# Kernel optimization log

Measured on AMD Instinct MI355X. Metric: run time of the kernel, lower is better.

Reference implementation:

```python
import jax, jax.numpy as jnp
import numpy as np

JACCARD_THRESH = 0.5
NEG_POS = 3
VAR0, VAR1 = 0.1, 0.2
MAX_POS = 256  # static cap on gathered positives for the metric-learning terms


def point_form(boxes):
    # (cx,cy,w,h) -> (xmin,ymin,xmax,ymax)
    return jnp.concatenate([boxes[:, :2] - boxes[:, 2:] / 2,
                            boxes[:, :2] + boxes[:, 2:] / 2], axis=1)


def jaccard(a, b):
    # a: [O,4], b: [D,4] point form
    lt = jnp.maximum(a[:, None, :2], b[None, :, :2])
    rb = jnp.minimum(a[:, None, 2:], b[None, :, 2:])
    wh = jnp.clip(rb - lt, 0.0)
    inter = wh[..., 0] * wh[..., 1]
    area_a = (a[:, 2] - a[:, 0]) * (a[:, 3] - a[:, 1])
    area_b = (b[:, 2] - b[:, 0]) * (b[:, 3] - b[:, 1])
    return inter / (area_a[:, None] + area_b[None, :] - inter)


def encode(matched, priors):
    g_cxcy = ((matched[:, :2] + matched[:, 2:]) / 2 - priors[:, :2]) / (VAR0 * priors[:, 2:])
    g_wh = jnp.log((matched[:, 2:] - matched[:, :2]) / priors[:, 2:]) / VAR1
    return jnp.concatenate([g_cxcy, g_wh], axis=1)


def match_one(truths, labels, poses, priors):
    # standard SSD match (per image)
    ov = jaccard(truths, point_form(priors))          # [O, D]
    best_prior_idx = jnp.argmax(ov, axis=1)           # [O]
    best_truth_ov = jnp.max(ov, axis=0)               # [D]
    best_truth_idx = jnp.argmax(ov, axis=0)           # [D]
    best_truth_ov = best_truth_ov.at[best_prior_idx].set(2.0)
    best_truth_idx = best_truth_idx.at[best_prior_idx].set(jnp.arange(truths.shape[0]))
    matches = truths[best_truth_idx]                  # [D,4]
    conf = labels[best_truth_idx] + 1                 # background=0
    conf = jnp.where(best_truth_ov < JACCARD_THRESH, 0, conf)
    return encode(matches, priors), conf.astype(jnp.int32), poses[best_truth_idx]


def multibox_loss(loc_data, conf_data, line_data, pose_data, dbox_list, targets):
    B, D, C = conf_data.shape
    truths = targets[:, :, 0:4]
    labels = targets[:, :, 4].astype(jnp.int32)
    poses = targets[:, :, 5:8]
    loc_t, conf_t, pose_t = jax.vmap(match_one, in_axes=(0, 0, 0, None))(
        truths, labels, poses, dbox_list)

    pos = conf_t > 0                                  # [B,D]
    posf = pos.astype(loc_data.dtype)

    # smooth-L1 loc loss over positives (sum reduction)
    d = loc_data - loc_t
    sl1 = jnp.where(jnp.abs(d) < 1.0, 0.5 * d * d, jnp.abs(d) - 0.5)
    loss_l = jnp.sum(sl1 * posf[..., None])

    # pose squared-error over positives
    loss_p = jnp.sum((pose_data - pose_t) ** 2 * posf[..., None])

    # per-anchor cross entropy + hard-negative mining (double-argsort rank trick)
    logp = jax.nn.log_softmax(conf_data, axis=-1)
    ce = -jnp.take_along_axis(logp, conf_t[..., None], axis=-1)[..., 0]  # [B,D]
    ce_mined = jnp.where(pos, 0.0, ce)
    loss_idx = jnp.argsort(-ce_mined, axis=1)
    idx_rank = jnp.argsort(loss_idx, axis=1)
    num_pos = jnp.sum(pos.astype(jnp.int32), axis=1, keepdims=True)
    num_neg = jnp.minimum(num_pos * NEG_POS, D)
    neg = idx_rank < num_neg
    loss_c = jnp.sum(ce * (pos | neg).astype(ce.dtype))

    N = jnp.maximum(jnp.sum(posf), 1.0)
    loss_l = loss_l / N
    loss_c = loss_c / N
    loss_p = loss_p / N

    # ---- metric-learning block on gathered positives (static cap) ----
    pos_flat = pos.reshape(-1)
    order = jnp.argsort(jnp.where(pos_flat, 0, 1))[:MAX_POS]  # stable: row-major positives first
    valid = pos_flat[order]                                   # [K]
    emb = line_data.reshape(-1, line_data.shape[-1])[order]   # [K,32] raw embeddings
    lab = conf_t.reshape(-1)[order]                           # [K]
    qp = pose_t.reshape(-1, 3)[order]                         # [K,3]

    # PairMarginMiner / TripletMarginLoss use L2-normalized LpDistance by default
    nemb = emb / jnp.maximum(jnp.linalg.norm(emb, axis=1, keepdims=True), 1e-12)
    sq = jnp.sum((nemb[:, None, :] - nemb[None, :, :]) ** 2, axis=-1)
    dist = jnp.sqrt(jnp.maximum(sq, 1e-12))                   # [K,K]

    K = emb.shape[0]
    eye = jnp.eye(K, dtype=bool)
    vpair = valid[:, None] & valid[None, :] & ~eye
    same = lab[:, None] == lab[None, :]
    pos_pair = vpair & same & (dist > 0.2)   # mined hard positive pairs
    neg_pair = vpair & ~same & (dist < 0.8)  # mined hard negative pairs
    n_pp = jnp.sum(pos_pair)
    n_np = jnp.sum(neg_pair)

    # pairs -> triplets sharing the anchor; TripletMarginLoss(margin=0.2), AvgNonZero reducer
    trip_mask = pos_pair[:, :, None] & neg_pair[:, None, :]           # [K,K,K]
    trip_loss = jax.nn.relu(dist[:, :, None] - dist[:, None, :] + 0.2)
    nz = trip_mask & (trip_loss > 0)
    loss_t = jnp.sum(jnp.where(nz, trip_loss, 0.0)) / jnp.maximum(jnp.sum(nz), 1)

    # Ldesk over mined positive pairs: raw-embedding sq-dist vs pose sq-dist consistency
    e_sq = jnp.sum((emb[:, None, :] - emb[None, :, :]) ** 2, axis=-1)
    q_sq = jnp.sum((qp[:, None, :] - qp[None, :, :]) ** 2, axis=-1)
    desk_sum = jnp.sum(jnp.where(pos_pair, (e_sq - q_sq) ** 2, 0.0))
    npp = jnp.maximum(n_pp, 1).astype(loc_data.dtype)
    Ldesk = desk_sum / npp + loss_t / jnp.maximum(n_pp + n_np, 1)
    Ldesk = Ldesk / npp / 32.0

    return loss_l, loss_c, loss_p, Ldesk, loss_t


def setup_inputs():
    key = jax.random.key(0)
    ks = jax.random.split(key, 10)
    B, D, C, L, O = 32, 8732, 21, 32, 8
    loc_data = jax.random.normal(ks[0], (B, D, 4)) * 0.1
    conf_data = jax.random.normal(ks[1], (B, D, C))
    line_data = jax.random.normal(ks[2], (B, D, L))
    pose_data = jax.random.normal(ks[3], (B, D, 3))
    # default boxes (cx,cy,w,h) in (0,1)
    cxcy = jax.random.uniform(ks[4], (D, 2), minval=0.05, maxval=0.95)
    wh = jax.random.uniform(ks[5], (D, 2), minval=0.05, maxval=0.4)
    dbox_list = jnp.concatenate([cxcy, wh], axis=1)
    # targets: [xmin,ymin,xmax,ymax,label,pose(3),unused]
    mins = jax.random.uniform(ks[6], (B, O, 2), minval=0.0, maxval=0.6)
    sizes = jax.random.uniform(ks[7], (B, O, 2), minval=0.1, maxval=0.4)
    boxes = jnp.concatenate([mins, mins + sizes], axis=-1)
    labs = jax.random.randint(ks[8], (B, O, 1), 0, C - 1).astype(jnp.float32)
    pz = jax.random.normal(ks[9], (B, O, 3))
    targets = jnp.concatenate([boxes, labs, pz, jnp.zeros((B, O, 1))], axis=-1)
    return dict(loc_data=loc_data, conf_data=conf_data, line_data=line_data,
                pose_data=pose_data, dbox_list=dbox_list, targets=targets)


def reference(loc_data, conf_data, line_data, pose_data, dbox_list, targets):
    return multibox_loss(loc_data, conf_data, line_data, pose_data, dbox_list, targets)
```

## Files before the change

### kernel.cpp

```cpp
#include <hip/hip_runtime.h>
#include <cstdint>

#define B 32
#define D 8732
#define C 21
#define L 32
#define O 8
#define NS 8
#define SLICE 1092
#define NT 1024

struct Ws {
  const float *loc, *conf, *line, *pose, *dbox, *targets;
  float* out;
  int* cnt;
  int* posSlice;
  float* sce;
  double *gLossL, *gLossP, *gCeP;
  double *gCeNeg;
  double *gDesk, *gNpp, *gNnp, *gTripS, *gTripC;
};

__device__ inline double waveSumD(double v) {
  #pragma unroll
  for (int s = 32; s > 0; s >>= 1) v += __shfl_down(v, s, 64);
  return v;
}

__device__ inline float iou_one(float tx1, float ty1, float tx2, float ty2, float ta,
                                float px1, float py1, float px2, float py2, float areaB) {
  float lx = fmaxf(tx1, px1), ly = fmaxf(ty1, py1);
  float rx = fminf(tx2, px2), ry = fminf(ty2, py2);
  float iw = fmaxf(rx - lx, 0.f), ih = fmaxf(ry - ly, 0.f);
  float inter = iw * ih;
  return inter / (ta + areaB - inter);
}

struct Sh1 {
  float tb[O][4], ta[O], tl[O], tp_[O][3];
  unsigned long long wm[16][O];
  int bpd[O];
  int plist[256];
  int wcnt[16], wbase[16];
  double wred[16][3];
  int run;
};

__global__ __launch_bounds__(NT) void k_match(Ws p) {
  __shared__ Sh1 sh;
  int g = blockIdx.x, tid = threadIdx.x;
  int lane = tid & 63, wav = tid >> 6;
  int b = g >> 3, s = g & 7;
  int dBeg = s * SLICE;
  int dEnd = dBeg + SLICE; if (dEnd > D) dEnd = D;

  if (tid < O) {
    const float* tr = p.targets + ((size_t)b * O + tid) * 9;
    sh.tb[tid][0] = tr[0]; sh.tb[tid][1] = tr[1];
    sh.tb[tid][2] = tr[2]; sh.tb[tid][3] = tr[3];
    sh.ta[tid] = (tr[2] - tr[0]) * (tr[3] - tr[1]);
    sh.tl[tid] = tr[4];
    sh.tp_[tid][0] = tr[5]; sh.tp_[tid][1] = tr[6]; sh.tp_[tid][2] = tr[7];
  }
  if (tid == 0) sh.run = 0;
  __syncthreads();

  {
    unsigned long long key[O];
    #pragma unroll
    for (int t = 0; t < O; t++) key[t] = 0ull;
    for (int d = tid; d < D; d += NT) {
      float4 db = *(const float4*)(p.dbox + (size_t)d * 4);
      float px1 = db.x - 0.5f*db.z, py1 = db.y - 0.5f*db.w;
      float px2 = db.x + 0.5f*db.z, py2 = db.y + 0.5f*db.w;
      float areaB = db.z * db.w;
      #pragma unroll
      for (int t = 0; t < O; t++) {
        float iou = iou_one(sh.tb[t][0], sh.tb[t][1], sh.tb[t][2], sh.tb[t][3],
                            sh.ta[t], px1, py1, px2, py2, areaB);
        unsigned long long kk = ((unsigned long long)__float_as_uint(iou) << 32)
                              | (unsigned long long)(0xFFFFFFFFu - (unsigned)d);
        if (kk > key[t]) key[t] = kk;
      }
    }
    #pragma unroll
    for (int t = 0; t < O; t++) {
      unsigned long long k = key[t];
      #pragma unroll
      for (int sft = 32; sft > 0; sft >>= 1) {
        unsigned long long o = __shfl_down(k, sft, 64);
        if (o > k) k = o;
      }
      if (lane == 0) sh.wm[wav][t] = k;
    }
    __syncthreads();
    if (tid < O) {
      unsigned long long k = sh.wm[0][tid];
      #pragma unroll
      for (int w = 1; w < 16; w++) if (sh.wm[w][tid] > k) k = sh.wm[w][tid];
      sh.bpd[tid] = (int)(0xFFFFFFFFu - (unsigned)(k & 0xFFFFFFFFull));
    }
    __syncthreads();
  }

  const unsigned long long lt = (lane == 0) ? 0ull : (~0ull >> (64 - lane));
  double ll = 0, lp = 0, cp = 0;
  for (int d0 = dBeg; d0 < dEnd; d0 += NT) {
    int d = d0 + tid;
    bool act = d < dEnd;
    int cls = 0, bi = 0;
    if (act) {
      float4 db = *(const float4*)(p.dbox + (size_t)d * 4);
      float px1 = db.x - 0.5f*db.z, py1 = db.y - 0.5f*db.w;
      float px2 = db.x + 0.5f*db.z, py2 = db.y + 0.5f*db.w;
      float areaB = db.z * db.w;
      float bv = -1.0f;
      #pragma unroll
      for (int t = 0; t < O; t++) {
        float iou = iou_one(sh.tb[t][0], sh.tb[t][1], sh.tb[t][2], sh.tb[t][3],
                            sh.ta[t], px1, py1, px2, py2, areaB);
        if (iou > bv) { bv = iou; bi = t; }
      }
      #pragma unroll
      for (int t = O - 1; t >= 0; t--)
        if (sh.bpd[t] == d) { bi = t; bv = 2.0f; break; }
      cls = (bv < 0.5f) ? 0 : ((int)sh.tl[bi] + 1);
      const float* cb = p.conf + ((size_t)b * D + d) * C;
      float x[C];
      #pragma unroll
      for (int c = 0; c < C; c++) x[c] = cb[c];
      float m = x[0];
      #pragma unroll
      for (int c = 1; c < C; c++) m = fmaxf(m, x[c]);
      float sm = 0.f;
      #pragma unroll
      for (int c = 0; c < C; c++) sm += __expf(x[c] - m);
      float xc = x[0];
      #pragma unroll
      for (int c = 1; c < C; c++) xc = (cls == c) ? x[c] : xc;
      float ce = m + __logf(sm) - xc;
      size_t bd = (size_t)b * D + d;
      if (cls > 0) {
        cp += ce;
        p.sce[bd] = 0.f;
        float g0 = ((sh.tb[bi][0] + sh.tb[bi][2]) * 0.5f - db.x) / (0.1f * db.z);
        float g1 = ((sh.tb[bi][1] + sh.tb[bi][3]) * 0.5f - db.y) / (0.1f * db.w);
        float g2 = logf((sh.tb[bi][2] - sh.tb[bi][0]) / db.z) / 0.2f;
        float g3 = logf((sh.tb[bi][3] - sh.tb[bi][1]) / db.w) / 0.2f;
        float4 lo = *(const float4*)(p.loc + bd * 4);
        float dv, a;
        dv = lo.x - g0; a = fabsf(dv); ll += (double)((a < 1.f) ? 0.5f*dv*dv : a - 0.5f);
        dv = lo.y - g1; a = fabsf(dv); ll += (double)((a < 1.f) ? 0.5f*dv*dv : a - 0.5f);
        dv = lo.z - g2; a = fabsf(dv); ll += (double)((a < 1.f) ? 0.5f*dv*dv : a - 0.5f);
        dv = lo.w - g3; a = fabsf(dv); ll += (double)((a < 1.f) ? 0.5f*dv*dv : a - 0.5f);
        const float* po = p.pose + bd * 3;
        #pragma unroll
        for (int q = 0; q < 3; q++) {
          float pd = po[q] - sh.tp_[bi][q];
          lp += (double)pd * (double)pd;
        }
      } else {
        p.sce[bd] = fmaxf(ce, 0.f);
      }
    }
    bool pos = act && (cls > 0);
    unsigned long long mm = __ballot(pos);
    if (lane == 0) sh.wcnt[wav] = __popcll(mm);
    __syncthreads();
    if (tid == 0) {
      int r = sh.run;
      #pragma unroll
      for (int w = 0; w < 16; w++) { sh.wbase[w] = r; r += sh.wcnt[w]; }
      sh.run = r;
    }
    __syncthreads();
    if (pos) {
      int rank = sh.wbase[wav] + __popcll(mm & lt);
      if (rank < 256) sh.plist[rank] = d | (cls << 14) | (bi << 19);
    }
    __syncthreads();
  }
  int tot = sh.run;
  if (tid == 0) p.cnt[g] = tot;
  int stored = (tot < 256) ? tot : 256;
  if (tid < stored) p.posSlice[g * 256 + tid] = sh.plist[tid];
  double a0 = waveSumD(ll), a1 = waveSumD(lp), a2 = waveSumD(cp);
  if (lane == 0) { sh.wred[wav][0] = a0; sh.wred[wav][1] = a1; sh.wred[wav][2] = a2; }
  __syncthreads();
  if (tid == 0) {
    double tll = 0, tlp = 0, tcp = 0;
    #pragma unroll
    for (int w = 0; w < 16; w++) { tll += sh.wred[w][0]; tlp += sh.wred[w][1]; tcp += sh.wred[w][2]; }
    p.gLossL[g] = tll; p.gLossP[g] = tlp; p.gCeP[g] = tcp;
  }
}

struct __align__(16) ShT {
  float sce[D];
  int whist[16][256];
  int hist[256];
  int scb[NS];
  int nposS;
  unsigned prefixSh; int kkSh;
  double wsum[16], wcnt2[16];
};
struct ShP {
  float embT[L][256];
  float nembT[L][256];
  float qp_s[256][3];
  int   lab_s[256];
  float sd[256];
  int   Pi[257];
  int   wscan[4];
  unsigned long long spm[4], snm[4];
  double w1[4];
  int ppc[4], npc[4];
  double wS[16], wC[16];
};
union Sh2 { ShT t; ShP pr; };

__global__ __launch_bounds__(NT) void k_mine(Ws p) {
  __shared__ Sh2 sh;
  int g = blockIdx.x, tid = threadIdx.x;
  int lane = tid & 63, wav = tid >> 6;

  if (g < B) {
    int bb = g;
    if (tid < NS) sh.t.scb[tid] = p.cnt[bb * NS + tid];
    const float* ce = p.sce + (size_t)bb * D;
    for (int i = tid; i < D / 4; i += NT)
      ((float4*)sh.t.sce)[i] = ((const float4*)ce)[i];
    __syncthreads();
    if (tid == 0) {
      int np = 0;
      #pragma unroll
      for (int q = 0; q < NS; q++) np += sh.t.scb[q];
      sh.t.nposS = np;
    }
    __syncthreads();
    int npos = sh.t.nposS;
    int k = npos * 3; if (k > D) k = D;
    unsigned prefix = 0; int kk = k;
    for (int pass = 0; pass < 4; pass++) {
      int shift = 24 - 8 * pass;
      for (int i = tid; i < 16 * 256; i += NT) ((int*)sh.t.whist)[i] = 0;
      __syncthreads();
      unsigned himask = (pass == 0) ? 0u : (0xFFFFFFFFu << (shift + 8));
      for (int d = tid; d < D; d += NT) {
        unsigned keyb = __float_as_uint(sh.t.sce[d]);
        if ((keyb & himask) == (prefix & himask))
          atomicAdd(&sh.t.whist[wav][(keyb >> shift) & 255], 1);
      }
      __syncthreads();
      if (tid < 256) {
        int h = 0;
        #pragma unroll
        for (int w = 0; w < 16; w++) h += sh.t.whist[w][tid];
        sh.t.hist[tid] = h;
      }
      __syncthreads();
      if (tid < 64) {
        int l = tid;
        int h0 = sh.t.hist[l*4], h1 = sh.t.hist[l*4+1], h2 = sh.t.hist[l*4+2], h3 = sh.t.hist[l*4+3];
        int loc4 = h0 + h1 + h2 + h3;
        int suf = loc4;
        #pragma unroll
        for (int st = 1; st < 64; st <<= 1) {
          int o = __shfl_down(suf, st, 64);
          if (l + st < 64) suf += o;
        }
        int snext = suf - loc4;
        int s3 = snext + h3, s2 = s3 + h2, s1 = s2 + h1, s0 = s1 + h0;
        if (s3 >= kk && snext < kk) { sh.t.prefixSh = prefix | ((unsigned)(l*4+3) << shift); sh.t.kkSh = kk - snext; }
        if (s2 >= kk && s3 < kk)    { sh.t.prefixSh = prefix | ((unsigned)(l*4+2) << shift); sh.t.kkSh = kk - s3; }
        if (s1 >= kk && s2 < kk)    { sh.t.prefixSh = prefix | ((unsigned)(l*4+1) << shift); sh.t.kkSh = kk - s2; }
        if (s0 >= kk && s1 < kk)    { sh.t.prefixSh = prefix | ((unsigned)(l*4+0) << shift); sh.t.kkSh = kk - s1; }
      }
      __syncthreads();
      prefix = sh.t.prefixSh; kk = sh.t.kkSh;
      __syncthreads();
    }
    float T = __uint_as_float(prefix);
    double sgt = 0.0; int cgt = 0;
    for (int d = tid; d < D; d += NT) {
      float v = sh.t.sce[d];
      if (__float_as_uint(v) > prefix) { sgt += (double)v; cgt++; }
    }
    double wv = waveSumD(sgt);
    double wc = waveSumD((double)cgt);
    if (lane == 0) { sh.t.wsum[wav] = wv; sh.t.wcnt2[wav] = wc; }
    __syncthreads();
    if (tid == 0) {
      double tsg = 0, tcg = 0;
      #pragma unroll
      for (int w = 0; w < 16; w++) { tsg += sh.t.wsum[w]; tcg += sh.t.wcnt2[w]; }
      p.gCeNeg[bb] = tsg + ((double)k - tcg) * (double)T;
    }
  } else {
    int i = g - B;
    int qq = tid >> 8, j = tid & 255;

    int v = (tid < 256) ? p.cnt[tid] : 0;
    #pragma unroll
    for (int st = 1; st < 64; st <<= 1) {
      int o = __shfl_up(v, st, 64);
      if (lane >= st) v += o;
    }
    if (tid < 256 && lane == 63) sh.pr.wscan[tid >> 6] = v;
    __syncthreads();
    if (tid < 256) {
      int add = 0;
      for (int q = 0; q < (tid >> 6); q++) add += sh.pr.wscan[q];
      sh.pr.Pi[tid + 1] = v + add;
    }
    if (tid == 0) sh.pr.Pi[0] = 0;
    __syncthreads();
    int total = sh.pr.Pi[256];
    int Pc = (total < 256) ? total : 256;

    if (tid < 256) {
      int slot = tid;
      bool val = slot < Pc;
      int cls = 0, dpr = 0, seg = 0;
      float q0 = 0.f, q1 = 0.f, q2 = 0.f;
      if (val) {
        int lo = 0;
        #pragma unroll
        for (int st = 128; st > 0; st >>= 1) {
          int m = lo + st;
          if (m <= 255 && sh.pr.Pi[m] <= slot) lo = m;
        }
        seg = lo;
        int idx = slot - sh.pr.Pi[seg];
        if (idx < 256) {
          int packed = p.posSlice[seg * 256 + idx];
          dpr = packed & 0x3FFF;
          cls = (packed >> 14) & 31;
          int bi = (packed >> 19) & 7;
          int bb2 = seg >> 3;
          const float* tr = p.targets + ((size_t)bb2 * O + bi) * 9;
          q0 = tr[5]; q1 = tr[6]; q2 = tr[7];
        } else val = false;
      }
      float nrm2 = 0.f;
      if (val) {
        int bb2 = seg >> 3;
        const float4* e4 = (const float4*)(p.line + ((size_t)bb2 * D + dpr) * L);
        #pragma unroll
        for (int c = 0; c < 8; c++) {
          float4 t4 = e4[c];
          sh.pr.embT[c*4+0][slot] = t4.x; sh.pr.embT[c*4+1][slot] = t4.y;
          sh.pr.embT[c*4+2][slot] = t4.z; sh.pr.embT[c*4+3][slot] = t4.w;
          nrm2 += t4.x*t4.x + t4.y*t4.y + t4.z*t4.z + t4.w*t4.w;
        }
      } else {
        #pragma unroll
        for (int c = 0; c < L; c++) sh.pr.embT[c][slot] = 0.f;
      }
      float inv = 1.f / fmaxf(sqrtf(nrm2), 1e-12f);
      #pragma unroll
      for (int c = 0; c < L; c++) sh.pr.nembT[c][slot] = sh.pr.embT[c][slot] * inv;
      sh.pr.lab_s[slot] = val ? cls : 0;
      sh.pr.qp_s[slot][0] = q0; sh.pr.qp_s[slot][1] = q1; sh.pr.qp_s[slot][2] = q2;
    }
    __syncthreads();

    int li = sh.pr.lab_s[i];
    bool vi = (i < Pc);
    bool pp = false, np = false;
    double dsk = 0.0;
    if (qq == 0) {
      bool vj = (j < Pc);
      float sq = 0.f, esq = 0.f;
      #pragma unroll
      for (int c = 0; c < 8; c++) {
        float d0 = sh.pr.nembT[c*4+0][i] - sh.pr.nembT[c*4+0][j];
        float d1 = sh.pr.nembT[c*4+1][i] - sh.pr.nembT[c*4+1][j];
        float d2 = sh.pr.nembT[c*4+2][i] - sh.pr.nembT[c*4+2][j];
        float d3 = sh.pr.nembT[c*4+3][i] - sh.pr.nembT[c*4+3][j];
        sq += d0*d0 + d1*d1 + d2*d2 + d3*d3;
        float e0 = sh.pr.embT[c*4+0][i] - sh.pr.embT[c*4+0][j];
        float e1 = sh.pr.embT[c*4+1][i] - sh.pr.embT[c*4+1][j];
        float e2 = sh.pr.embT[c*4+2][i] - sh.pr.embT[c*4+2][j];
        float e3 = sh.pr.embT[c*4+3][i] - sh.pr.embT[c*4+3][j];
        esq += e0*e0 + e1*e1 + e2*e2 + e3*e3;
      }
      float dd = sqrtf(fmaxf(sq, 1e-12f));
      sh.pr.sd[j] = dd;
      float qsq = 0.f;
      #pragma unroll
      for (int c = 0; c < 3; c++) {
        float dq = sh.pr.qp_s[i][c] - sh.pr.qp_s[j][c];
        qsq += dq * dq;
      }
      bool vp = vi && vj && (i != j);
      bool same = (li == sh.pr.lab_s[j]);
      pp = vp && same && (dd > 0.2f);
      np = vp && !same && (dd < 0.8f);
      float diff = esq - qsq;
      dsk = pp ? (double)diff * (double)diff : 0.0;
    }
    unsigned long long pb = __ballot(pp), nb = __ballot(np);
    double dw = waveSumD(dsk);
    if (lane == 0 && wav < 4) {
      sh.pr.spm[wav] = pb; sh.pr.snm[wav] = nb; sh.pr.w1[wav] = dw;
      sh.pr.ppc[wav] = (int)__popcll(pb); sh.pr.npc[wav] = (int)__popcll(nb);
    }
    __syncthreads();
    unsigned long long pmw = sh.pr.spm[j >> 6];
    bool pj = (pmw >> (j & 63)) & 1ull;
    float sdj = sh.pr.sd[j];
    double ts = 0.0, tc = 0.0;
    if (pj) {
      for (int it = 0; it < 64; it++) {
        int kx = qq + 4 * it;
        unsigned long long nmw = sh.pr.snm[kx >> 6];
        if ((nmw >> (kx & 63)) & 1ull) {
          float x = sdj - sh.pr.sd[kx] + 0.2f;
          if (x > 0.f) { ts += (double)x; tc += 1.0; }
        }
      }
    }
    ts = waveSumD(ts); tc = waveSumD(tc);
    if (lane == 0) { sh.pr.wS[wav] = ts; sh.pr.wC[wav] = tc; }
    __syncthreads();
    if (tid == 0) {
      double S = 0, Cc = 0;
      #pragma unroll
      for (int w = 0; w < 16; w++) { S += sh.pr.wS[w]; Cc += sh.pr.wC[w]; }
      double dsum = sh.pr.w1[0] + sh.pr.w1[1] + sh.pr.w1[2] + sh.pr.w1[3];
      int pcnt = sh.pr.ppc[0] + sh.pr.ppc[1] + sh.pr.ppc[2] + sh.pr.ppc[3];
      int ncnt = sh.pr.npc[0] + sh.pr.npc[1] + sh.pr.npc[2] + sh.pr.npc[3];
      p.gDesk[i] = dsum; p.gNpp[i] = (double)pcnt; p.gNnp[i] = (double)ncnt;
      p.gTripS[i] = S; p.gTripC[i] = Cc;
    }
  }
}

__global__ __launch_bounds__(256) void k_fin(Ws p) {
  __shared__ double lbuf[4];
  int tid = threadIdx.x;
  auto sumD = [&](const double* a, int n) -> double {
    double v = 0;
    for (int i = tid; i < n; i += 256) v += a[i];
    v = waveSumD(v);
    __syncthreads();
    if ((tid & 63) == 0) lbuf[tid >> 6] = v;
    __syncthreads();
    double r = lbuf[0] + lbuf[1] + lbuf[2] + lbuf[3];
    __syncthreads();
    return r;
  };
  double lossL = sumD(p.gLossL, 256);
  double lossP = sumD(p.gLossP, 256);
  double ceP   = sumD(p.gCeP,   256);
  double ceN   = sumD(p.gCeNeg,  B);
  double desk  = sumD(p.gDesk,  256);
  double npp   = sumD(p.gNpp,   256);
  double nnp   = sumD(p.gNnp,   256);
  double tripS = sumD(p.gTripS, 256);
  double tripC = sumD(p.gTripC, 256);
  double Ntot;
  {
    double v = 0;
    for (int i = tid; i < 256; i += 256) v += (double)p.cnt[i];
    v = waveSumD(v);
    __syncthreads();
    if ((tid & 63) == 0) lbuf[tid >> 6] = v;
    __syncthreads();
    Ntot = lbuf[0] + lbuf[1] + lbuf[2] + lbuf[3];
  }
  if (tid == 0) {
    double N = (Ntot > 0.0) ? Ntot : 1.0;
    p.out[0] = (float)(lossL / N);
    p.out[1] = (float)((ceP + ceN) / N);
    p.out[2] = (float)(lossP / N);
    double cnt = (tripC > 0.0) ? tripC : 1.0;
    double loss_t = tripS / cnt;
    double nppd = (npp > 0.0) ? npp : 1.0;
    double tot = npp + nnp;
    double denom = (tot > 0.0) ? tot : 1.0;
    double Ldesk = desk / nppd + loss_t / denom;
    Ldesk = Ldesk / nppd / 32.0;
    p.out[3] = (float)Ldesk;
    p.out[4] = (float)loss_t;
  }
}

extern "C" void kernel_launch(void* const* d_in, const int* in_sizes, int n_in,
                              void* d_out, int out_size, void* d_ws, size_t ws_size,
                              hipStream_t stream) {
  char* ws = (char*)d_ws;
  size_t off = 0;
  auto alloc = [&](size_t bytes) -> char* {
    char* q = ws + off;
    off += (bytes + 255) & ~(size_t)255;
    return q;
  };
  Ws p;
  p.loc     = (const float*)d_in[0];
  p.conf    = (const float*)d_in[1];
  p.line    = (const float*)d_in[2];
  p.pose    = (const float*)d_in[3];
  p.dbox    = (const float*)d_in[4];
  p.targets = (const float*)d_in[5];
  p.out     = (float*)d_out;
  p.cnt      = (int*)alloc(256 * 4);
  p.posSlice = (int*)alloc(256 * 256 * 4);
  p.sce      = (float*)alloc((size_t)B * D * 4);
  p.gLossL   = (double*)alloc(256 * 8);
  p.gLossP   = (double*)alloc(256 * 8);
  p.gCeP     = (double*)alloc(256 * 8);
  p.gCeNeg   = (double*)alloc(B * 8);
  p.gDesk    = (double*)alloc(256 * 8);
  p.gNpp     = (double*)alloc(256 * 8);
  p.gNnp     = (double*)alloc(256 * 8);
  p.gTripS   = (double*)alloc(256 * 8);
  p.gTripC   = (double*)alloc(256 * 8);

  k_match<<<256,     NT, 0, stream>>>(p);
  k_mine <<<256 + B, NT, 0, stream>>>(p);
  k_fin  <<<1,      256, 0, stream>>>(p);
}
```

Baseline: 150.6 us.

## Split best-prior search into separate kernel, shrink match slices, fuse final reduction

Result: slower. 215.1 us (+42.9%).

```diff
diff --git a/kernel.cpp b/kernel.cpp
--- a/kernel.cpp
+++ b/kernel.cpp
@@ -6,13 +6,20 @@
 #define C 21
 #define L 32
 #define O 8
-#define NS 8
-#define SLICE 1092
+#define NSEGB 16
+#define SEGLEN 546
+#define NSEG 512
+#define MT 576
 #define NT 1024
+#define PAIRB 128
+#define TOPB 32
+#define FINTGT (PAIRB + TOPB)
 
 struct Ws {
   const float *loc, *conf, *line, *pose, *dbox, *targets;
   float* out;
+  unsigned long long* bpPart;
+  int* finCtr;
   int* cnt;
   int* posSlice;
   float* sce;
@@ -36,24 +43,82 @@
   return inter / (ta + areaB - inter);
 }
 
-struct Sh1 {
+__global__ __launch_bounds__(256) void k_bp(Ws p) {
+  __shared__ float tb[O][4], ta[O];
+  __shared__ unsigned long long wm[4][O];
+  int g = blockIdx.x, tid = threadIdx.x;
+  int lane = tid & 63, wav = tid >> 6;
+  int b = g >> 4, s = g & 15;
+  int dBeg = s * SEGLEN;
+  int dEnd = dBeg + SEGLEN; if (dEnd > D) dEnd = D;
+  if (g == 0 && tid == 0) *p.finCtr = 0;
+  if (tid < O) {
+    const float* tr = p.targets + ((size_t)b * O + tid) * 9;
+    tb[tid][0] = tr[0]; tb[tid][1] = tr[1]; tb[tid][2] = tr[2]; tb[tid][3] = tr[3];
+    ta[tid] = (tr[2] - tr[0]) * (tr[3] - tr[1]);
+  }
+  __syncthreads();
+  float bi_[O]; int bd_[O];
+  #pragma unroll
+  for (int t = 0; t < O; t++) { bi_[t] = 0.f; bd_[t] = 0; }
+  for (int d = dBeg + tid; d < dEnd; d += 256) {
+    float4 db = *(const float4*)(p.dbox + (size_t)d * 4);
+    float px1 = db.x - 0.5f*db.z, py1 = db.y - 0.5f*db.w;
+    float px2 = db.x + 0.5f*db.z, py2 = db.y + 0.5f*db.w;
+    float areaB = db.z * db.w;
+    #pragma unroll
+    for (int t = 0; t < O; t++) {
+      float iou = iou_one(tb[t][0], tb[t][1], tb[t][2], tb[t][3], ta[t],
+                          px1, py1, px2, py2, areaB);
+      if (iou > bi_[t]) { bi_[t] = iou; bd_[t] = d; }
+    }
+  }
+  #pragma unroll
+  for (int t = 0; t < O; t++) {
+    unsigned long long k = ((unsigned long long)__float_as_uint(bi_[t]) << 32)
+                         | (unsigned long long)(0xFFFFFFFFu - (unsigned)bd_[t]);
+    #pragma unroll
+    for (int sft = 32; sft > 0; sft >>= 1) {
+      unsigned long long o = __shfl_down(k, sft, 64);
+      if (o > k) k = o;
+    }
+    if (lane == 0) wm[wav][t] = k;
+  }
+  __syncthreads();
+  if (tid < O) {
+    unsigned long long k = wm[0][tid];
+    #pragma unroll
+    for (int w = 1; w < 4; w++) if (wm[w][tid] > k) k = wm[w][tid];
+    p.bpPart[(size_t)g * O + tid] = k;
+  }
+}
+
+struct ShM {
   float tb[O][4], ta[O], tl[O], tp_[O][3];
-  unsigned long long wm[16][O];
+  unsigned long long bpred[128];
   int bpd[O];
   int plist[256];
-  int wcnt[16], wbase[16];
-  double wred[16][3];
+  int wcnt[9], wbase[9];
+  double wred[9][3];
   int run;
 };
 
-__global__ __launch_bounds__(NT) void k_match(Ws p) {
-  __shared__ Sh1 sh;
+__global__ __launch_bounds__(MT, 4) void k_match(Ws p) {
+  __shared__ ShM sh;
   int g = blockIdx.x, tid = threadIdx.x;
   int lane = tid & 63, wav = tid >> 6;
-  int b = g >> 3, s = g & 7;
-  int dBeg = s * SLICE;
-  int dEnd = dBeg + SLICE; if (dEnd > D) dEnd = D;
-
+  int b = g >> 4, s = g & 15;
+  int dBeg = s * SEGLEN;
+  int dEnd = dBeg + SEGLEN; if (dEnd > D) dEnd = D;
+  int d = dBeg + tid;
+  bool act = d < dEnd;
+
+  float x[C];
+  if (act) {
+    const float* cb = p.conf + ((size_t)b * D + d) * C;
+    #pragma unroll
+    for (int c = 0; c < C; c++) x[c] = cb[c];
+  }
   if (tid < O) {
     const float* tr = p.targets + ((size_t)b * O + tid) * 9;
     sh.tb[tid][0] = tr[0]; sh.tb[tid][1] = tr[1];
@@ -62,124 +127,90 @@
     sh.tl[tid] = tr[4];
     sh.tp_[tid][0] = tr[5]; sh.tp_[tid][1] = tr[6]; sh.tp_[tid][2] = tr[7];
   }
-  if (tid == 0) sh.run = 0;
-  __syncthreads();
-
-  {
-    unsigned long long key[O];
-    #pragma unroll
-    for (int t = 0; t < O; t++) key[t] = 0ull;
-    for (int d = tid; d < D; d += NT) {
-      float4 db = *(const float4*)(p.dbox + (size_t)d * 4);
-      float px1 = db.x - 0.5f*db.z, py1 = db.y - 0.5f*db.w;
-      float px2 = db.x + 0.5f*db.z, py2 = db.y + 0.5f*db.w;
-      float areaB = db.z * db.w;
-      #pragma unroll
-      for (int t = 0; t < O; t++) {
-        float iou = iou_one(sh.tb[t][0], sh.tb[t][1], sh.tb[t][2], sh.tb[t][3],
-                            sh.ta[t], px1, py1, px2, py2, areaB);
-        unsigned long long kk = ((unsigned long long)__float_as_uint(iou) << 32)
-                              | (unsigned long long)(0xFFFFFFFFu - (unsigned)d);
-        if (kk > key[t]) key[t] = kk;
-      }
-    }
+  if (tid < 128)
+    sh.bpred[tid] = p.bpPart[((size_t)b * NSEGB + (tid >> 3)) * O + (tid & 7)];
+  __syncthreads();
+  if (tid < O) {
+    unsigned long long k = 0ull;
+    #pragma unroll
+    for (int s2 = 0; s2 < NSEGB; s2++) {
+      unsigned long long kk = sh.bpred[s2 * 8 + tid];
+      if (kk > k) k = kk;
+    }
+    sh.bpd[tid] = (int)(0xFFFFFFFFu - (unsigned)(k & 0xFFFFFFFFull));
+  }
+  __syncthreads();
+
+  double ll = 0, lp = 0, cp = 0;
+  int cls = 0, bi = 0;
+  if (act) {
+    float4 db = *(const float4*)(p.dbox + (size_t)d * 4);
+    float px1 = db.x - 0.5f*db.z, py1 = db.y - 0.5f*db.w;
+    float px2 = db.x + 0.5f*db.z, py2 = db.y + 0.5f*db.w;
+    float areaB = db.z * db.w;
+    float bv = -1.0f;
     #pragma unroll
     for (int t = 0; t < O; t++) {
-      unsigned long long k = key[t];
-      #pragma unroll
-      for (int sft = 32; sft > 0; sft >>= 1) {
-        unsigned long long o = __shfl_down(k, sft, 64);
-        if (o > k) k = o;
-      }
-      if (lane == 0) sh.wm[wav][t] = k;
-    }
-    __syncthreads();
-    if (tid < O) {
-      unsigned long long k = sh.wm[0][tid];
-      #pragma unroll
-      for (int w = 1; w < 16; w++) if (sh.wm[w][tid] > k) k = sh.wm[w][tid];
-      sh.bpd[tid] = (int)(0xFFFFFFFFu - (unsigned)(k & 0xFFFFFFFFull));
-    }
-    __syncthreads();
+      float iou = iou_one(sh.tb[t][0], sh.tb[t][1], sh.tb[t][2], sh.tb[t][3],
+                          sh.ta[t], px1, py1, px2, py2, areaB);
+      if (iou > bv) { bv = iou; bi = t; }
+    }
+    #pragma unroll
+    for (int t = O - 1; t >= 0; t--)
+      if (sh.bpd[t] == d) { bi = t; bv = 2.0f; break; }
+    cls = (bv < 0.5f) ? 0 : ((int)sh.tl[bi] + 1);
+    float m = x[0];
+    #pragma unroll
+    for (int c = 1; c < C; c++) m = fmaxf(m, x[c]);
+    float sm = 0.f;
+    #pragma unroll
+    for (int c = 0; c < C; c++) sm += __expf(x[c] - m);
+    float xc = x[0];
+    #pragma unroll
+    for (int c = 1; c < C; c++) xc = (cls == c) ? x[c] : xc;
+    float ce = m + __logf(sm) - xc;
+    size_t bd = (size_t)b * D + d;
+    if (cls > 0) {
+      cp += ce;
+      p.sce[bd] = 0.f;
+      float g0 = ((sh.tb[bi][0] + sh.tb[bi][2]) * 0.5f - db.x) / (0.1f * db.z);
+      float g1 = ((sh.tb[bi][1] + sh.tb[bi][3]) * 0.5f - db.y) / (0.1f * db.w);
+      float g2 = logf((sh.tb[bi][2] - sh.tb[bi][0]) / db.z) / 0.2f;
+      float g3 = logf((sh.tb[bi][3] - sh.tb[bi][1]) / db.w) / 0.2f;
+      float4 lo = *(const float4*)(p.loc + bd * 4);
+      float dv, a;
+      dv = lo.x - g0; a = fabsf(dv); ll += (double)((a < 1.f) ? 0.5f*dv*dv : a - 0.5f);
+      dv = lo.y - g1; a = fabsf(dv); ll += (double)((a < 1.f) ? 0.5f*dv*dv : a - 0.5f);
+      dv = lo.z - g2; a = fabsf(dv); ll += (double)((a < 1.f) ? 0.5f*dv*dv : a - 0.5f);
+      dv = lo.w - g3; a = fabsf(dv); ll += (double)((a < 1.f) ? 0.5f*dv*dv : a - 0.5f);
+      const float* po = p.pose + bd * 3;
+      #pragma unroll
+      for (int q = 0; q < 3; q++) {
+        float pd = po[q] - sh.tp_[bi][q];
+        lp += (double)pd * (double)pd;
+      }
+    } else {
+      p.sce[bd] = fmaxf(ce, 0.f);
+    }
   }
 
   const unsigned long long lt = (lane == 0) ? 0ull : (~0ull >> (64 - lane));
-  double ll = 0, lp = 0, cp = 0;
-  for (int d0 = dBeg; d0 < dEnd; d0 += NT) {
-    int d = d0 + tid;
-    bool act = d < dEnd;
-    int cls = 0, bi = 0;
-    if (act) {
-      float4 db = *(const float4*)(p.dbox + (size_t)d * 4);
-      float px1 = db.x - 0.5f*db.z, py1 = db.y - 0.5f*db.w;
-      float px2 = db.x + 0.5f*db.z, py2 = db.y + 0.5f*db.w;
-      float areaB = db.z * db.w;
-      float bv = -1.0f;
-      #pragma unroll
-      for (int t = 0; t < O; t++) {
-        float iou = iou_one(sh.tb[t][0], sh.tb[t][1], sh.tb[t][2], sh.tb[t][3],
-                            sh.ta[t], px1, py1, px2, py2, areaB);
-        if (iou > bv) { bv = iou; bi = t; }
-      }
-      #pragma unroll
-      for (int t = O - 1; t >= 0; t--)
-        if (sh.bpd[t] == d) { bi = t; bv = 2.0f; break; }
-      cls = (bv < 0.5f) ? 0 : ((int)sh.tl[bi] + 1);
-      const float* cb = p.conf + ((size_t)b * D + d) * C;
-      float x[C];
-      #pragma unroll
-      for (int c = 0; c < C; c++) x[c] = cb[c];
-      float m = x[0];
-      #pragma unroll
-      for (int c = 1; c < C; c++) m = fmaxf(m, x[c]);
-      float sm = 0.f;
-      #pragma unroll
-      for (int c = 0; c < C; c++) sm += __expf(x[c] - m);
-      float xc = x[0];
-      #pragma unroll
-      for (int c = 1; c < C; c++) xc = (cls == c) ? x[c] : xc;
-      float ce = m + __logf(sm) - xc;
-      size_t bd = (size_t)b * D + d;
-      if (cls > 0) {
-        cp += ce;
-        p.sce[bd] = 0.f;
-        float g0 = ((sh.tb[bi][0] + sh.tb[bi][2]) * 0.5f - db.x) / (0.1f * db.z);
-        float g1 = ((sh.tb[bi][1] + sh.tb[bi][3]) * 0.5f - db.y) / (0.1f * db.w);
-        float g2 = logf((sh.tb[bi][2] - sh.tb[bi][0]) / db.z) / 0.2f;
-        float g3 = logf((sh.tb[bi][3] - sh.tb[bi][1]) / db.w) / 0.2f;
-        float4 lo = *(const float4*)(p.loc + bd * 4);
-        float dv, a;
-        dv = lo.x - g0; a = fabsf(dv); ll += (double)((a < 1.f) ? 0.5f*dv*dv : a - 0.5f);
-        dv = lo.y - g1; a = fabsf(dv); ll += (double)((a < 1.f) ? 0.5f*dv*dv : a - 0.5f);
-        dv = lo.z - g2; a = fabsf(dv); ll += (double)((a < 1.f) ? 0.5f*dv*dv : a - 0.5f);
-        dv = lo.w - g3; a = fabsf(dv); ll += (double)((a < 1.f) ? 0.5f*dv*dv : a - 0.5f);
-        const float* po = p.pose + bd * 3;
-        #pragma unroll
-        for (int q = 0; q < 3; q++) {
-          float pd = po[q] - sh.tp_[bi][q];
-          lp += (double)pd * (double)pd;
-        }
-      } else {
-        p.sce[bd] = fmaxf(ce, 0.f);
-      }
-    }
-    bool pos = act && (cls > 0);
-    unsigned long long mm = __ballot(pos);
-    if (lane == 0) sh.wcnt[wav] = __popcll(mm);
-    __syncthreads();
-    if (tid == 0) {
-      int r = sh.run;
-      #pragma unroll
-      for (int w = 0; w < 16; w++) { sh.wbase[w] = r; r += sh.wcnt[w]; }
-      sh.run = r;
-    }
-    __syncthreads();
-    if (pos) {
-      int rank = sh.wbase[wav] + __popcll(mm & lt);
-      if (rank < 256) sh.plist[rank] = d | (cls << 14) | (bi << 19);
-    }
-    __syncthreads();
-  }
+  bool pos = act && (cls > 0);
+  unsigned long long mm = __ballot(pos);
+  if (lane == 0) sh.wcnt[wav] = __popcll(mm);
+  __syncthreads();
+  if (tid == 0) {
+    int r = 0;
+    #pragma unroll
+    for (int w = 0; w < 9; w++) { sh.wbase[w] = r; r += sh.wcnt[w]; }
+    sh.run = r;
+  }
+  __syncthreads();
+  if (pos) {
+    int rank = sh.wbase[wav] + __popcll(mm & lt);
+    if (rank < 256) sh.plist[rank] = d | (cls << 14) | (bi << 19);
+  }
+  __syncthreads();
   int tot = sh.run;
   if (tid == 0) p.cnt[g] = tot;
   int stored = (tot < 256) ? tot : 256;
@@ -190,7 +221,7 @@
   if (tid == 0) {
     double tll = 0, tlp = 0, tcp = 0;
     #pragma unroll
-    for (int w = 0; w < 16; w++) { tll += sh.wred[w][0]; tlp += sh.wred[w][1]; tcp += sh.wred[w][2]; }
+    for (int w = 0; w < 9; w++) { tll += sh.wred[w][0]; tlp += sh.wred[w][1]; tcp += sh.wred[w][2]; }
     p.gLossL[g] = tll; p.gLossP[g] = tlp; p.gCeP[g] = tcp;
   }
 }
@@ -199,7 +230,7 @@
   float sce[D];
   int whist[16][256];
   int hist[256];
-  int scb[NS];
+  int scb[NSEGB];
   int nposS;
   unsigned prefixSh; int kkSh;
   double wsum[16], wcnt2[16];
@@ -209,24 +240,25 @@
   float nembT[L][256];
   float qp_s[256][3];
   int   lab_s[256];
-  float sd[256];
-  int   Pi[257];
-  int   wscan[4];
-  unsigned long long spm[4], snm[4];
-  double w1[4];
-  int ppc[4], npc[4];
+  float sd[2][256];
+  int   Pi[NSEG + 1];
+  int   wscan[8];
+  unsigned long long spm[2][4], snm[2][4];
+  double w1[2][4];
+  int ppc[2][4], npc[2][4];
   double wS[16], wC[16];
 };
-union Sh2 { ShT t; ShP pr; };
-
-__global__ __launch_bounds__(NT) void k_mine(Ws p) {
+struct ShD { double lbuf[16]; int last; };
+union Sh2 { ShT t; ShP pr; ShD dd; };
+
+__global__ __launch_bounds__(NT) void k_minefin(Ws p) {
   __shared__ Sh2 sh;
   int g = blockIdx.x, tid = threadIdx.x;
   int lane = tid & 63, wav = tid >> 6;
 
-  if (g < B) {
-    int bb = g;
-    if (tid < NS) sh.t.scb[tid] = p.cnt[bb * NS + tid];
+  if (g >= PAIRB) {
+    int bb = g - PAIRB;
+    if (tid < NSEGB) sh.t.scb[tid] = p.cnt[bb * NSEGB + tid];
     const float* ce = p.sce + (size_t)bb * D;
     for (int i = tid; i < D / 4; i += NT)
       ((float4*)sh.t.sce)[i] = ((const float4*)ce)[i];
@@ -234,7 +266,7 @@
     if (tid == 0) {
       int np = 0;
       #pragma unroll
-      for (int q = 0; q < NS; q++) np += sh.t.scb[q];
+      for (int q = 0; q < NSEGB; q++) np += sh.t.scb[q];
       sh.t.nposS = np;
     }
     __syncthreads();
@@ -297,25 +329,26 @@
       p.gCeNeg[bb] = tsg + ((double)k - tcg) * (double)T;
     }
   } else {
-    int i = g - B;
-    int qq = tid >> 8, j = tid & 255;
-
-    int v = (tid < 256) ? p.cnt[tid] : 0;
+    int rgrp = tid >> 9;
+    int i = 2 * g + rgrp;
+    int t5 = tid & 511, j = t5 & 255, qq = t5 >> 8;
+
+    int v = (tid < NSEG) ? p.cnt[tid] : 0;
     #pragma unroll
     for (int st = 1; st < 64; st <<= 1) {
       int o = __shfl_up(v, st, 64);
       if (lane >= st) v += o;
     }
-    if (tid < 256 && lane == 63) sh.pr.wscan[tid >> 6] = v;
-    __syncthreads();
-    if (tid < 256) {
+    if (tid < NSEG && lane == 63) sh.pr.wscan[tid >> 6] = v;
+    __syncthreads();
+    if (tid < NSEG) {
       int add = 0;
       for (int q = 0; q < (tid >> 6); q++) add += sh.pr.wscan[q];
       sh.pr.Pi[tid + 1] = v + add;
     }
     if (tid == 0) sh.pr.Pi[0] = 0;
     __syncthreads();
-    int total = sh.pr.Pi[256];
+    int total = sh.pr.Pi[NSEG];
     int Pc = (total < 256) ? total : 256;
 
     if (tid < 256) {
@@ -326,9 +359,9 @@
       if (val) {
         int lo = 0;
         #pragma unroll
-        for (int st = 128; st > 0; st >>= 1) {
+        for (int st = 256; st > 0; st >>= 1) {
           int m = lo + st;
-          if (m <= 255 && sh.pr.Pi[m] <= slot) lo = m;
+          if (m <= NSEG - 1 && sh.pr.Pi[m] <= slot) lo = m;
         }
         seg = lo;
         int idx = slot - sh.pr.Pi[seg];
@@ -337,14 +370,14 @@
           dpr = packed & 0x3FFF;
           cls = (packed >> 14) & 31;
           int bi = (packed >> 19) & 7;
-          int bb2 = seg >> 3;
+          int bb2 = seg >> 4;
           const float* tr = p.targets + ((size_t)bb2 * O + bi) * 9;
           q0 = tr[5]; q1 = tr[6]; q2 = tr[7];
         } else val = false;
       }
       float nrm2 = 0.f;
       if (val) {
-        int bb2 = seg >> 3;
+        int bb2 = seg >> 4;
         const float4* e4 = (const float4*)(p.line + ((size_t)bb2 * D + dpr) * L);
         #pragma unroll
         for (int c = 0; c < 8; c++) {
@@ -373,20 +406,14 @@
       bool vj = (j < Pc);
       float sq = 0.f, esq = 0.f;
       #pragma unroll
-      for (int c = 0; c < 8; c++) {
-        float d0 = sh.pr.nembT[c*4+0][i] - sh.pr.nembT[c*4+0][j];
-        float d1 = sh.pr.nembT[c*4+1][i] - sh.pr.nembT[c*4+1][j];
-        float d2 = sh.pr.nembT[c*4+2][i] - sh.pr.nembT[c*4+2][j];
-        float d3 = sh.pr.nembT[c*4+3][i] - sh.pr.nembT[c*4+3][j];
-        sq += d0*d0 + d1*d1 + d2*d2 + d3*d3;
-        float e0 = sh.pr.embT[c*4+0][i] - sh.pr.embT[c*4+0][j];
-        float e1 = sh.pr.embT[c*4+1][i] - sh.pr.embT[c*4+1][j];
-        float e2 = sh.pr.embT[c*4+2][i] - sh.pr.embT[c*4+2][j];
-        float e3 = sh.pr.embT[c*4+3][i] - sh.pr.embT[c*4+3][j];
-        esq += e0*e0 + e1*e1 + e2*e2 + e3*e3;
-      }
-      float dd = sqrtf(fmaxf(sq, 1e-12f));
-      sh.pr.sd[j] = dd;
+      for (int c = 0; c < L; c++) {
+        float dn = sh.pr.nembT[c][i] - sh.pr.nembT[c][j];
+        sq += dn * dn;
+        float de = sh.pr.embT[c][i] - sh.pr.embT[c][j];
+        esq += de * de;
+      }
+      float ddv = sqrtf(fmaxf(sq, 1e-12f));
+      sh.pr.sd[rgrp][j] = ddv;
       float qsq = 0.f;
       #pragma unroll
       for (int c = 0; c < 3; c++) {
@@ -395,95 +422,108 @@
       }
       bool vp = vi && vj && (i != j);
       bool same = (li == sh.pr.lab_s[j]);
-      pp = vp && same && (dd > 0.2f);
-      np = vp && !same && (dd < 0.8f);
+      pp = vp && same && (ddv > 0.2f);
+      np = vp && !same && (ddv < 0.8f);
       float diff = esq - qsq;
       dsk = pp ? (double)diff * (double)diff : 0.0;
     }
     unsigned long long pb = __ballot(pp), nb = __ballot(np);
     double dw = waveSumD(dsk);
-    if (lane == 0 && wav < 4) {
-      sh.pr.spm[wav] = pb; sh.pr.snm[wav] = nb; sh.pr.w1[wav] = dw;
-      sh.pr.ppc[wav] = (int)__popcll(pb); sh.pr.npc[wav] = (int)__popcll(nb);
-    }
-    __syncthreads();
-    unsigned long long pmw = sh.pr.spm[j >> 6];
+    if (lane == 0 && qq == 0) {
+      int w4 = wav & 3;
+      sh.pr.spm[rgrp][w4] = pb; sh.pr.snm[rgrp][w4] = nb; sh.pr.w1[rgrp][w4] = dw;
+      sh.pr.ppc[rgrp][w4] = (int)__popcll(pb); sh.pr.npc[rgrp][w4] = (int)__popcll(nb);
+    }
+    __syncthreads();
+    unsigned long long pmw = sh.pr.spm[rgrp][j >> 6];
     bool pj = (pmw >> (j & 63)) & 1ull;
-    float sdj = sh.pr.sd[j];
+    float sdj = sh.pr.sd[rgrp][j];
     double ts = 0.0, tc = 0.0;
     if (pj) {
-      for (int it = 0; it < 64; it++) {
-        int kx = qq + 4 * it;
-        unsigned long long nmw = sh.pr.snm[kx >> 6];
+      for (int it = 0; it < 128; it++) {
+        int kx = qq + 2 * it;
+        unsigned long long nmw = sh.pr.snm[rgrp][kx >> 6];
         if ((nmw >> (kx & 63)) & 1ull) {
-          float x = sdj - sh.pr.sd[kx] + 0.2f;
-          if (x > 0.f) { ts += (double)x; tc += 1.0; }
+          float xv = sdj - sh.pr.sd[rgrp][kx] + 0.2f;
+          if (xv > 0.f) { ts += (double)xv; tc += 1.0; }
         }
       }
     }
     ts = waveSumD(ts); tc = waveSumD(tc);
     if (lane == 0) { sh.pr.wS[wav] = ts; sh.pr.wC[wav] = tc; }
     __syncthreads();
-    if (tid == 0) {
+    if (tid == 0 || tid == 512) {
+      int r = rgrp;
       double S = 0, Cc = 0;
       #pragma unroll
-      for (int w = 0; w < 16; w++) { S += sh.pr.wS[w]; Cc += sh.pr.wC[w]; }
-      double dsum = sh.pr.w1[0] + sh.pr.w1[1] + sh.pr.w1[2] + sh.pr.w1[3];
-      int pcnt = sh.pr.ppc[0] + sh.pr.ppc[1] + sh.pr.ppc[2] + sh.pr.ppc[3];
-      int ncnt = sh.pr.npc[0] + sh.pr.npc[1] + sh.pr.npc[2] + sh.pr.npc[3];
+      for (int w = 0; w < 8; w++) { S += sh.pr.wS[r * 8 + w]; Cc += sh.pr.wC[r * 8 + w]; }
+      double dsum = sh.pr.w1[r][0] + sh.pr.w1[r][1] + sh.pr.w1[r][2] + sh.pr.w1[r][3];
+      int pcnt = sh.pr.ppc[r][0] + sh.pr.ppc[r][1] + sh.pr.ppc[r][2] + sh.pr.ppc[r][3];
+      int ncnt = sh.pr.npc[r][0] + sh.pr.npc[r][1] + sh.pr.npc[r][2] + sh.pr.npc[r][3];
       p.gDesk[i] = dsum; p.gNpp[i] = (double)pcnt; p.gNnp[i] = (double)ncnt;
       p.gTripS[i] = S; p.gTripC[i] = Cc;
     }
   }
-}
-
-__global__ __launch_bounds__(256) void k_fin(Ws p) {
-  __shared__ double lbuf[4];
-  int tid = threadIdx.x;
-  auto sumD = [&](const double* a, int n) -> double {
-    double v = 0;
-    for (int i = tid; i < n; i += 256) v += a[i];
-    v = waveSumD(v);
-    __syncthreads();
-    if ((tid & 63) == 0) lbuf[tid >> 6] = v;
-    __syncthreads();
-    double r = lbuf[0] + lbuf[1] + lbuf[2] + lbuf[3];
-    __syncthreads();
-    return r;
-  };
-  double lossL = sumD(p.gLossL, 256);
-  double lossP = sumD(p.gLossP, 256);
-  double ceP   = sumD(p.gCeP,   256);
-  double ceN   = sumD(p.gCeNeg,  B);
-  double desk  = sumD(p.gDesk,  256);
-  double npp   = sumD(p.gNpp,   256);
-  double nnp   = sumD(p.gNnp,   256);
-  double tripS = sumD(p.gTripS, 256);
-  double tripC = sumD(p.gTripC, 256);
-  double Ntot;
+
+  __threadfence();
+  __syncthreads();
+  if (tid == 0) {
+    int prev = __hip_atomic_fetch_add(p.finCtr, 1, __ATOMIC_ACQ_REL, __HIP_MEMORY_SCOPE_AGENT);
+    sh.dd.last = (prev == FINTGT - 1);
+  }
+  __syncthreads();
+  if (!sh.dd.last) return;
+  __threadfence();
   {
-    double v = 0;
-    for (int i = tid; i < 256; i += 256) v += (double)p.cnt[i];
-    v = waveSumD(v);
-    __syncthreads();
-    if ((tid & 63) == 0) lbuf[tid >> 6] = v;
-    __syncthreads();
-    Ntot = lbuf[0] + lbuf[1] + lbuf[2] + lbuf[3];
-  }
-  if (tid == 0) {
-    double N = (Ntot > 0.0) ? Ntot : 1.0;
-    p.out[0] = (float)(lossL / N);
-    p.out[1] = (float)((ceP + ceN) / N);
-    p.out[2] = (float)(lossP / N);
-    double cnt = (tripC > 0.0) ? tripC : 1.0;
-    double loss_t = tripS / cnt;
-    double nppd = (npp > 0.0) ? npp : 1.0;
-    double tot = npp + nnp;
-    double denom = (tot > 0.0) ? tot : 1.0;
-    double Ldesk = desk / nppd + loss_t / denom;
-    Ldesk = Ldesk / nppd / 32.0;
-    p.out[3] = (float)Ldesk;
-    p.out[4] = (float)loss_t;
+    auto sumD = [&](const double* a, int n) -> double {
+      double v = 0;
+      for (int i = tid; i < n; i += NT) v += a[i];
+      v = waveSumD(v);
+      __syncthreads();
+      if (lane == 0) sh.dd.lbuf[wav] = v;
+      __syncthreads();
+      double r = 0;
+      #pragma unroll
+      for (int w = 0; w < 16; w++) r += sh.dd.lbuf[w];
+      __syncthreads();
+      return r;
+    };
+    double lossL = sumD(p.gLossL, NSEG);
+    double lossP = sumD(p.gLossP, NSEG);
+    double ceP   = sumD(p.gCeP,   NSEG);
+    double ceN   = sumD(p.gCeNeg,  B);
+    double desk  = sumD(p.gDesk,  256);
+    double npp   = sumD(p.gNpp,   256);
+    double nnp   = sumD(p.gNnp,   256);
+    double tripS = sumD(p.gTripS, 256);
+    double tripC = sumD(p.gTripC, 256);
+    double Ntot;
+    {
+      double v = 0;
+      for (int i = tid; i < NSEG; i += NT) v += (double)p.cnt[i];
+      v = waveSumD(v);
+      __syncthreads();
+      if (lane == 0) sh.dd.lbuf[wav] = v;
+      __syncthreads();
+      Ntot = 0;
+      #pragma unroll
+      for (int w = 0; w < 16; w++) Ntot += sh.dd.lbuf[w];
+    }
+    if (tid == 0) {
+      double N = (Ntot > 0.0) ? Ntot : 1.0;
+      p.out[0] = (float)(lossL / N);
+      p.out[1] = (float)((ceP + ceN) / N);
+      p.out[2] = (float)(lossP / N);
+      double cnt = (tripC > 0.0) ? tripC : 1.0;
+      double loss_t = tripS / cnt;
+      double nppd = (npp > 0.0) ? npp : 1.0;
+      double tot = npp + nnp;
+      double denom = (tot > 0.0) ? tot : 1.0;
+      double Ldesk = desk / nppd + loss_t / denom;
+      Ldesk = Ldesk / nppd / 32.0;
+      p.out[3] = (float)Ldesk;
+      p.out[4] = (float)loss_t;
+    }
   }
 }
 
@@ -505,12 +545,14 @@
   p.dbox    = (const float*)d_in[4];
   p.targets = (const float*)d_in[5];
   p.out     = (float*)d_out;
-  p.cnt      = (int*)alloc(256 * 4);
-  p.posSlice = (int*)alloc(256 * 256 * 4);
+  p.bpPart   = (unsigned long long*)alloc((size_t)NSEG * O * 8);
+  p.finCtr   = (int*)alloc(256);
+  p.cnt      = (int*)alloc(NSEG * 4);
+  p.posSlice = (int*)alloc((size_t)NSEG * 256 * 4);
   p.sce      = (float*)alloc((size_t)B * D * 4);
-  p.gLossL   = (double*)alloc(256 * 8);
-  p.gLossP   = (double*)alloc(256 * 8);
-  p.gCeP     = (double*)alloc(256 * 8);
+  p.gLossL   = (double*)alloc(NSEG * 8);
+  p.gLossP   = (double*)alloc(NSEG * 8);
+  p.gCeP     = (double*)alloc(NSEG * 8);
   p.gCeNeg   = (double*)alloc(B * 8);
   p.gDesk    = (double*)alloc(256 * 8);
   p.gNpp     = (double*)alloc(256 * 8);
@@ -518,7 +560,7 @@
   p.gTripS   = (double*)alloc(256 * 8);
   p.gTripC   = (double*)alloc(256 * 8);
 
-  k_match<<<256,     NT, 0, stream>>>(p);
-  k_mine <<<256 + B, NT, 0, stream>>>(p);
-  k_fin  <<<1,      256, 0, stream>>>(p);
+  k_bp     <<<NSEG,  256, 0, stream>>>(p);
+  k_match  <<<NSEG,  MT,  0, stream>>>(p);
+  k_minefin<<<FINTGT, NT, 0, stream>>>(p);
 }
```
